# Kernel tuning notes

Hardware: AMD Instinct MI355X
Metric: run time of the kernel (lower is better)

## Reference

```python
import jax, jax.numpy as jnp
import numpy as np

B, T, C = 2, 2048, 1024
N_HEAD = 16
HEAD = C // N_HEAD  # 64


def setup_inputs() -> dict:
    key = jax.random.key(0)
    k1, k2, k3, k4, k5 = jax.random.split(key, 5)
    s = 1.0 / np.sqrt(C)
    return {
        "x": jax.random.normal(k1, (B, T, C), dtype=jnp.float32),
        "w_qkv": jax.random.normal(k2, (C, 3 * C), dtype=jnp.float32) * s,
        "b_qkv": jax.random.normal(k3, (3 * C,), dtype=jnp.float32) * 0.01,
        "w_proj": jax.random.normal(k4, (C, C), dtype=jnp.float32) * s,
        "b_proj": jax.random.normal(k5, (C,), dtype=jnp.float32) * 0.01,
    }


def reference(x, w_qkv, b_qkv, w_proj, b_proj):
    b, t, c = x.shape
    # QKV projection -> (3, B, H, T, head)
    qkv = (x @ w_qkv + b_qkv).reshape(b, t, 3, N_HEAD, HEAD).transpose(2, 0, 3, 1, 4)
    q, k, v = qkv[0], qkv[1], qkv[2]
    # scaled causal attention scores [B,H,T,T]
    att = jnp.einsum("bhqd,bhkd->bhqk", q, k) * (HEAD ** -0.5)
    causal = jnp.tril(jnp.ones((t, t), dtype=bool))
    att = jnp.where(causal, att, jnp.float32(-jnp.inf))
    att = jax.nn.softmax(att, axis=-1)
    out = jnp.einsum("bhqk,bhkd->bhqd", att, v)  # [B,H,T,head]
    out = out.transpose(0, 2, 1, 3).reshape(b, t, c)
    # dropout is identity in eval mode (p effectively 0)
    return out @ w_proj + b_proj
```

## Files before the change

kernel.cpp:

```cpp
#include <hip/hip_runtime.h>
#include <cstdint>

typedef __attribute__((ext_vector_type(8))) short bf16x8_t;
typedef __attribute__((ext_vector_type(4))) float f32x4_t;
typedef __attribute__((ext_vector_type(16))) float f32x16_t;

#define T_SEQ 2048
#define NHEAD 16
#define CDIM  1024

__device__ __forceinline__ unsigned short f2bf(float f) {
  union { float f; unsigned u; } v; v.f = f;
  unsigned r = v.u + 0x7FFFu + ((v.u >> 16) & 1u);
  return (unsigned short)(r >> 16);
}

__device__ __forceinline__ float fast_exp2(float x) {
#if __has_builtin(__builtin_amdgcn_exp2f)
  return __builtin_amdgcn_exp2f(x);
#else
  return __expf(x * 0.6931471805599453f);
#endif
}

__device__ __forceinline__ unsigned cvtpk(float lo, float hi) {
  unsigned r;
  asm("v_cvt_pk_bf16_f32 %0, %1, %2" : "=v"(r) : "v"(lo), "v"(hi));
  return r;
}
#define PLSWAP(a, b) asm("v_permlane32_swap_b32 %0, %1" : "+v"(a), "+v"(b))

__device__ __forceinline__ void gload_lds16(const void* g, void* l) {
  typedef const uint32_t __attribute__((address_space(1)))* gp_t;
  typedef uint32_t __attribute__((address_space(3)))* lp_t;
  __builtin_amdgcn_global_load_lds((gp_t)(uintptr_t)g, (lp_t)(uint32_t)(uintptr_t)l, 16, 0, 0);
}

__global__ void conv_bf16_kernel(const float* __restrict__ in,
                                 unsigned short* __restrict__ out, int n4) {
  int i = blockIdx.x * blockDim.x + threadIdx.x;
  if (i >= n4) return;
  float4 v = ((const float4*)in)[i];
  ushort4 o;
  o.x = f2bf(v.x); o.y = f2bf(v.y); o.z = f2bf(v.z); o.w = f2bf(v.w);
  ((ushort4*)out)[i] = o;
}

__global__ void transpose_bf16_kernel(const float* __restrict__ W,
                                      unsigned short* __restrict__ WT, int R, int C) {
  __shared__ unsigned short tile[64][65];
  const int c0 = blockIdx.x * 64, r0 = blockIdx.y * 64;
  const int t = threadIdx.x;
  #pragma unroll
  for (int i = 0; i < 16; i++) {
    int idx = i * 256 + t;
    int r = idx >> 6, c = idx & 63;
    tile[r][c] = f2bf(W[(size_t)(r0 + r) * C + c0 + c]);
  }
  __syncthreads();
  #pragma unroll
  for (int i = 0; i < 16; i++) {
    int idx = i * 256 + t;
    int c = idx >> 6, r = idx & 63;
    WT[(size_t)(c0 + c) * R + r0 + r] = tile[r][c];
  }
}

template <int MODE>
__global__ void gemm_bt_kernel(const unsigned short* __restrict__ A,
                               const unsigned short* __restrict__ Bt,
                               const float* __restrict__ bias,
                               unsigned short* __restrict__ q_out,
                               unsigned short* __restrict__ k_out,
                               unsigned short* __restrict__ v_out,
                               float* __restrict__ c_out,
                               int K, int N) {
  const int t = threadIdx.x;
  const int w = t >> 6, l = t & 63;
  const int lr = l & 15, lg = l >> 4;
  const int wr = w >> 1, wc = w & 1;
  const int m0 = blockIdx.y * 128, n0 = blockIdx.x * 128;

  __shared__ __align__(16) unsigned short As[128 * 64];
  __shared__ __align__(16) unsigned short Bs[128 * 64];

  f32x4_t acc[4][4];
  #pragma unroll
  for (int mi = 0; mi < 4; mi++)
    #pragma unroll
    for (int ni = 0; ni < 4; ni++)
      acc[mi][ni] = (f32x4_t){0.f, 0.f, 0.f, 0.f};

  const int srow = t >> 3;
  const int scol = (t & 7) * 8;
  const size_t abase = (size_t)(m0 + srow) * K + scol;
  const size_t bbase = (size_t)(n0 + srow) * K + scol;

  for (int k0 = 0; k0 < K; k0 += 64) {
    __syncthreads();
    #pragma unroll
    for (int i = 0; i < 4; i++) {
      gload_lds16(A + abase + (size_t)i * 32 * K + k0, &As[(i * 32 + srow) * 64 + scol]);
      gload_lds16(Bt + bbase + (size_t)i * 32 * K + k0, &Bs[(i * 32 + srow) * 64 + scol]);
    }
    __syncthreads();
    #pragma unroll
    for (int ks = 0; ks < 2; ks++) {
      bf16x8_t af[4], bfr[4];
      #pragma unroll
      for (int mi = 0; mi < 4; mi++)
        af[mi] = *(const bf16x8_t*)&As[(wr * 64 + mi * 16 + lr) * 64 + ks * 32 + lg * 8];
      #pragma unroll
      for (int ni = 0; ni < 4; ni++)
        bfr[ni] = *(const bf16x8_t*)&Bs[(wc * 64 + ni * 16 + lr) * 64 + ks * 32 + lg * 8];
      #pragma unroll
      for (int mi = 0; mi < 4; mi++)
        #pragma unroll
        for (int ni = 0; ni < 4; ni++)
          acc[mi][ni] = __builtin_amdgcn_mfma_f32_16x16x32_bf16(af[mi], bfr[ni], acc[mi][ni], 0, 0, 0);
    }
  }

  if (MODE == 0) {
    const float QSCALE = 0.125f * 1.4426950408889634f;
    #pragma unroll
    for (int ni = 0; ni < 4; ni++) {
      const int n = n0 + wc * 64 + ni * 16 + lr;
      const float bv = bias[n];
      const int s = n >> 10;
      const int hh = (n >> 6) & 15;
      const int d = n & 63;
      #pragma unroll
      for (int mi = 0; mi < 4; mi++) {
        const int mbase = m0 + wr * 64 + mi * 16 + lg * 4;
        const int batch = mbase >> 11;
        const int tt = mbase & 2047;
        const int bhh = batch * NHEAD + hh;
        if (s == 0) {
          #pragma unroll
          for (int r = 0; r < 4; r++)
            q_out[((size_t)bhh * T_SEQ + tt + r) * 64 + d] = f2bf((acc[mi][ni][r] + bv) * QSCALE);
        } else if (s == 1) {
          #pragma unroll
          for (int r = 0; r < 4; r++) {
            const int dsw = ((((d >> 3) ^ ((tt + r) & 7)) << 3) | (d & 7));
            k_out[((size_t)bhh * T_SEQ + tt + r) * 64 + dsw] = f2bf(acc[mi][ni][r] + bv);
          }
        } else {
          ushort4 pk;
          pk.x = f2bf(acc[mi][ni][0] + bv);
          pk.y = f2bf(acc[mi][ni][1] + bv);
          pk.z = f2bf(acc[mi][ni][2] + bv);
          pk.w = f2bf(acc[mi][ni][3] + bv);
          const int c2 = (((tt >> 3) & 7) ^ (d & 7));
          const int tt2 = (tt & ~63) | (c2 << 3) | (tt & 7);
          *(ushort4*)&v_out[((size_t)bhh * 64 + d) * T_SEQ + tt2] = pk;
        }
      }
    }
  } else {
    #pragma unroll
    for (int ni = 0; ni < 4; ni++) {
      const int n = n0 + wc * 64 + ni * 16 + lr;
      const float bv = bias[n];
      #pragma unroll
      for (int mi = 0; mi < 4; mi++) {
        const int m = m0 + wr * 64 + mi * 16 + lg * 4;
        #pragma unroll
        for (int r = 0; r < 4; r++)
          c_out[(size_t)(m + r) * N + n] = acc[mi][ni][r] + bv;
      }
    }
  }
}

__global__ __launch_bounds__(256, 2)
void attn_kernel(const unsigned short* __restrict__ Qb,
                 const unsigned short* __restrict__ Kswz,
                 const unsigned short* __restrict__ Vswz,
                 unsigned short* __restrict__ O) {
  const int b0 = blockIdx.x;
  const int xcd = b0 & 7;
  const int i = b0 >> 3;
  const int bh = xcd * 4 + (i & 3);
  const int strip = 15 - (i >> 2);
  const int batch = bh >> 4, h = bh & 15;
  const int q0 = strip * 128;
  const int nT = 2 * strip + 2;

  const int t = threadIdx.x;
  const int w = t >> 6, l = t & 63;
  const int q31 = l & 31, hi = l >> 5;

  __shared__ __align__(16) unsigned short Ks[2][64 * 64];
  __shared__ __align__(16) unsigned short Vs[2][64 * 64];

  const size_t kvbase = (size_t)bh * T_SEQ;

  auto stage = [&](int buf, int kv0) {
    #pragma unroll
    for (int i2 = 0; i2 < 2; i2++) {
      const int r0 = w * 16 + i2 * 8;
      gload_lds16(Kswz + (kvbase + kv0 + r0 + (l >> 3)) * 64 + (l & 7) * 8,
                  &Ks[buf][r0 * 64 + l * 8]);
      gload_lds16(Vswz + ((size_t)bh * 64 + r0 + (l >> 3)) * T_SEQ + kv0 + (l & 7) * 8,
                  &Vs[buf][r0 * 64 + l * 8]);
    }
  };

  bf16x8_t qf[4];
  #pragma unroll
  for (int ds = 0; ds < 4; ds++)
    qf[ds] = *(const bf16x8_t*)&Qb[(kvbase + q0 + w * 32 + q31) * 64 + ds * 16 + hi * 8];

  f32x16_t accO[2];
  #pragma unroll
  for (int di = 0; di < 2; di++)
    #pragma unroll
    for (int j = 0; j < 16; j++) accO[di][j] = 0.f;
  float l_part = 0.f;

  stage(0, 0);
  __syncthreads();
  int cur = 0;

  for (int ti = 0; ti < nT; ++ti) {
    if (ti + 1 < nT) stage(cur ^ 1, (ti + 1) * 64);

    const bool active = !(ti == nT - 1 && w < 2);
    if (active) {
      f32x16_t sc[2];
      #pragma unroll
      for (int c = 0; c < 2; c++)
        #pragma unroll
        for (int j = 0; j < 16; j++) sc[c][j] = 0.f;
      #pragma unroll
      for (int ds = 0; ds < 4; ds++) {
        #pragma unroll
        for (int c = 0; c < 2; c++) {
          const int row = c * 32 + q31;
          bf16x8_t ka = *(const bf16x8_t*)&Ks[cur][row * 64 + (((ds * 2 + hi) ^ (row & 7)) << 3)];
          sc[c] = __builtin_amdgcn_mfma_f32_32x32x16_bf16(ka, qf[ds], sc[c], 0, 0, 0);
        }
      }

      if ((ti == nT - 2 && w < 2) || (ti == nT - 1 && w >= 2)) {
        const int lb = (ti == nT - 1) ? 64 : 0;
        const int ql = w * 32 + q31;
        #pragma unroll
        for (int c = 0; c < 2; c++)
          #pragma unroll
          for (int r = 0; r < 16; r++) {
            const int kvl = lb + c * 32 + (r & 3) + 8 * (r >> 2) + 4 * hi;
            if (kvl > ql) sc[c][r] = -1e30f;
          }
      }

      #pragma unroll
      for (int c = 0; c < 2; c++) {
        float p[16];
        #pragma unroll
        for (int r = 0; r < 16; r++) {
          p[r] = fast_exp2(sc[c][r]);
          l_part += p[r];
        }
        unsigned pk0 = cvtpk(p[0], p[1]),   pk1 = cvtpk(p[2], p[3]);
        unsigned pk2 = cvtpk(p[4], p[5]),   pk3 = cvtpk(p[6], p[7]);
        unsigned pk4 = cvtpk(p[8], p[9]),   pk5 = cvtpk(p[10], p[11]);
        unsigned pk6 = cvtpk(p[12], p[13]), pk7 = cvtpk(p[14], p[15]);

        PLSWAP(pk0, pk2);
        PLSWAP(pk1, pk3);
        union { unsigned u[4]; bf16x8_t v; } pb0 = {{pk0, pk1, pk2, pk3}};
        {
          const int s = c * 2;
          #pragma unroll
          for (int di = 0; di < 2; di++) {
            const int row = di * 32 + q31;
            bf16x8_t va = *(const bf16x8_t*)&Vs[cur][row * 64 + (((s * 2 + hi) ^ (row & 7)) << 3)];
            accO[di] = __builtin_amdgcn_mfma_f32_32x32x16_bf16(va, pb0.v, accO[di], 0, 0, 0);
          }
        }
        PLSWAP(pk4, pk6);
        PLSWAP(pk5, pk7);
        union { unsigned u[4]; bf16x8_t v; } pb1 = {{pk4, pk5, pk6, pk7}};
        {
          const int s = c * 2 + 1;
          #pragma unroll
          for (int di = 0; di < 2; di++) {
            const int row = di * 32 + q31;
            bf16x8_t va = *(const bf16x8_t*)&Vs[cur][row * 64 + (((s * 2 + hi) ^ (row & 7)) << 3)];
            accO[di] = __builtin_amdgcn_mfma_f32_32x32x16_bf16(va, pb1.v, accO[di], 0, 0, 0);
          }
        }
      }
    }

    __syncthreads();
    cur ^= 1;
  }

  const float l_tot = l_part + __shfl_xor(l_part, 32);
  const float rl = 1.0f / l_tot;
  const int q = q0 + w * 32 + q31;
  unsigned short* orow = O + ((size_t)batch * T_SEQ + q) * CDIM + h * 64;
  #pragma unroll
  for (int di = 0; di < 2; di++)
    #pragma unroll
    for (int g = 0; g < 4; g++) {
      const unsigned w0 = cvtpk(accO[di][4 * g] * rl, accO[di][4 * g + 1] * rl);
      const unsigned w1 = cvtpk(accO[di][4 * g + 2] * rl, accO[di][4 * g + 3] * rl);
      const int d = di * 32 + 8 * g + 4 * hi;
      uint2 pr; pr.x = w0; pr.y = w1;
      *(uint2*)&orow[d] = pr;
    }
}

extern "C" void kernel_launch(void* const* d_in, const int* in_sizes, int n_in,
                              void* d_out, int out_size, void* d_ws, size_t ws_size,
                              hipStream_t stream) {
  (void)in_sizes; (void)n_in; (void)out_size; (void)ws_size;
  const float* x      = (const float*)d_in[0];
  const float* w_qkv  = (const float*)d_in[1];
  const float* b_qkv  = (const float*)d_in[2];
  const float* w_proj = (const float*)d_in[3];
  const float* b_proj = (const float*)d_in[4];
  float* out = (float*)d_out;

  char* ws = (char*)d_ws;
  unsigned short* xb     = (unsigned short*)(ws);
  unsigned short* wqkvT  = (unsigned short*)(ws + ((size_t)8  << 20));
  unsigned short* wprojT = (unsigned short*)(ws + ((size_t)14 << 20));
  unsigned short* qb     = (unsigned short*)(ws + ((size_t)16 << 20));
  unsigned short* kb     = (unsigned short*)(ws + ((size_t)24 << 20));
  unsigned short* vtb    = (unsigned short*)(ws + ((size_t)32 << 20));
  unsigned short* ab     = (unsigned short*)(ws + ((size_t)40 << 20));

  conv_bf16_kernel<<<4096, 256, 0, stream>>>(x, xb, (2 * T_SEQ * CDIM) / 4);
  transpose_bf16_kernel<<<dim3(48, 16), 256, 0, stream>>>(w_qkv, wqkvT, 1024, 3072);
  transpose_bf16_kernel<<<dim3(16, 16), 256, 0, stream>>>(w_proj, wprojT, 1024, 1024);
  gemm_bt_kernel<0><<<dim3(24, 32), 256, 0, stream>>>(xb, wqkvT, b_qkv, qb, kb, vtb, nullptr, 1024, 3072);
  attn_kernel<<<512, 256, 0, stream>>>(qb, kb, vtb, ab);
  gemm_bt_kernel<1><<<dim3(8, 32), 256, 0, stream>>>(ab, wprojT, b_proj, nullptr, nullptr, nullptr, out, 1024, 1024);
}
```

Before: 109.2 us.

## Shrink GEMM tiles, remap blocks per XCD, and raise occupancy

The QKV GEMM now uses 128x64 tiles and the output projection uses 64x64 tiles, replacing 128x128. Blocks are launched on a 1-D grid and remapped so each XCD works on a contiguous band of rows, which should improve L2 reuse. Launch bounds ask for higher occupancy and K is fixed at compile time. The aim is more blocks in flight and better latency hiding across the 256 CUs. The cost is less data reuse per tile and more redundant loads of the A and B tiles.

Measured after the change: 110.5 us. Within noise of the previous version (+1.1%).

```diff
diff --git a/kernel.cpp b/kernel.cpp
--- a/kernel.cpp
+++ b/kernel.cpp
@@ -67,28 +67,43 @@
 }
 
 template <int MODE>
-__global__ void gemm_bt_kernel(const unsigned short* __restrict__ A,
-                               const unsigned short* __restrict__ Bt,
-                               const float* __restrict__ bias,
-                               unsigned short* __restrict__ q_out,
-                               unsigned short* __restrict__ k_out,
-                               unsigned short* __restrict__ v_out,
-                               float* __restrict__ c_out,
-                               int K, int N) {
+__global__ __launch_bounds__(256, MODE == 0 ? 6 : 4)
+void gemm_bt_kernel(const unsigned short* __restrict__ A,
+                    const unsigned short* __restrict__ Bt,
+                    const float* __restrict__ bias,
+                    unsigned short* __restrict__ q_out,
+                    unsigned short* __restrict__ k_out,
+                    unsigned short* __restrict__ v_out,
+                    float* __restrict__ c_out) {
+  constexpr int TM = (MODE == 0) ? 128 : 64;
+  constexpr int FM = TM / 32;
+  constexpr int K = 1024;
+
   const int t = threadIdx.x;
   const int w = t >> 6, l = t & 63;
   const int lr = l & 15, lg = l >> 4;
   const int wr = w >> 1, wc = w & 1;
-  const int m0 = blockIdx.y * 128, n0 = blockIdx.x * 128;
-
-  __shared__ __align__(16) unsigned short As[128 * 64];
-  __shared__ __align__(16) unsigned short Bs[128 * 64];
-
-  f32x4_t acc[4][4];
-  #pragma unroll
-  for (int mi = 0; mi < 4; mi++)
-    #pragma unroll
-    for (int ni = 0; ni < 4; ni++)
+
+  const int b0 = blockIdx.x;
+  const int xcd = b0 & 7;
+  const int idx = b0 >> 3;
+  int m0, n0;
+  if (MODE == 0) {
+    m0 = (xcd * 4 + idx / 48) * 128;
+    n0 = (idx % 48) * 64;
+  } else {
+    m0 = (xcd * 8 + (idx >> 4)) * 64;
+    n0 = (idx & 15) * 64;
+  }
+
+  __shared__ __align__(16) unsigned short As[TM * 64];
+  __shared__ __align__(16) unsigned short Bs[64 * 64];
+
+  f32x4_t acc[FM][2];
+  #pragma unroll
+  for (int mi = 0; mi < FM; mi++)
+    #pragma unroll
+    for (int ni = 0; ni < 2; ni++)
       acc[mi][ni] = (f32x4_t){0.f, 0.f, 0.f, 0.f};
 
   const int srow = t >> 3;
@@ -99,24 +114,25 @@
   for (int k0 = 0; k0 < K; k0 += 64) {
     __syncthreads();
     #pragma unroll
-    for (int i = 0; i < 4; i++) {
+    for (int i = 0; i < TM / 32; i++)
       gload_lds16(A + abase + (size_t)i * 32 * K + k0, &As[(i * 32 + srow) * 64 + scol]);
+    #pragma unroll
+    for (int i = 0; i < 2; i++)
       gload_lds16(Bt + bbase + (size_t)i * 32 * K + k0, &Bs[(i * 32 + srow) * 64 + scol]);
-    }
     __syncthreads();
     #pragma unroll
     for (int ks = 0; ks < 2; ks++) {
-      bf16x8_t af[4], bfr[4];
-      #pragma unroll
-      for (int mi = 0; mi < 4; mi++)
-        af[mi] = *(const bf16x8_t*)&As[(wr * 64 + mi * 16 + lr) * 64 + ks * 32 + lg * 8];
-      #pragma unroll
-      for (int ni = 0; ni < 4; ni++)
-        bfr[ni] = *(const bf16x8_t*)&Bs[(wc * 64 + ni * 16 + lr) * 64 + ks * 32 + lg * 8];
-      #pragma unroll
-      for (int mi = 0; mi < 4; mi++)
-        #pragma unroll
-        for (int ni = 0; ni < 4; ni++)
+      bf16x8_t af[FM], bfr[2];
+      #pragma unroll
+      for (int mi = 0; mi < FM; mi++)
+        af[mi] = *(const bf16x8_t*)&As[(wr * (TM / 2) + mi * 16 + lr) * 64 + ks * 32 + lg * 8];
+      #pragma unroll
+      for (int ni = 0; ni < 2; ni++)
+        bfr[ni] = *(const bf16x8_t*)&Bs[(wc * 32 + ni * 16 + lr) * 64 + ks * 32 + lg * 8];
+      #pragma unroll
+      for (int mi = 0; mi < FM; mi++)
+        #pragma unroll
+        for (int ni = 0; ni < 2; ni++)
           acc[mi][ni] = __builtin_amdgcn_mfma_f32_16x16x32_bf16(af[mi], bfr[ni], acc[mi][ni], 0, 0, 0);
     }
   }
@@ -124,14 +140,14 @@
   if (MODE == 0) {
     const float QSCALE = 0.125f * 1.4426950408889634f;
     #pragma unroll
-    for (int ni = 0; ni < 4; ni++) {
-      const int n = n0 + wc * 64 + ni * 16 + lr;
+    for (int ni = 0; ni < 2; ni++) {
+      const int n = n0 + wc * 32 + ni * 16 + lr;
       const float bv = bias[n];
       const int s = n >> 10;
       const int hh = (n >> 6) & 15;
       const int d = n & 63;
       #pragma unroll
-      for (int mi = 0; mi < 4; mi++) {
+      for (int mi = 0; mi < FM; mi++) {
         const int mbase = m0 + wr * 64 + mi * 16 + lg * 4;
         const int batch = mbase >> 11;
         const int tt = mbase & 2047;
@@ -160,15 +176,15 @@
     }
   } else {
     #pragma unroll
-    for (int ni = 0; ni < 4; ni++) {
-      const int n = n0 + wc * 64 + ni * 16 + lr;
+    for (int ni = 0; ni < 2; ni++) {
+      const int n = n0 + wc * 32 + ni * 16 + lr;
       const float bv = bias[n];
       #pragma unroll
-      for (int mi = 0; mi < 4; mi++) {
-        const int m = m0 + wr * 64 + mi * 16 + lg * 4;
+      for (int mi = 0; mi < FM; mi++) {
+        const int m = m0 + wr * 32 + mi * 16 + lg * 4;
         #pragma unroll
         for (int r = 0; r < 4; r++)
-          c_out[(size_t)(m + r) * N + n] = acc[mi][ni][r] + bv;
+          c_out[(size_t)(m + r) * 1024 + n] = acc[mi][ni][r] + bv;
       }
     }
   }
@@ -339,7 +355,7 @@
   conv_bf16_kernel<<<4096, 256, 0, stream>>>(x, xb, (2 * T_SEQ * CDIM) / 4);
   transpose_bf16_kernel<<<dim3(48, 16), 256, 0, stream>>>(w_qkv, wqkvT, 1024, 3072);
   transpose_bf16_kernel<<<dim3(16, 16), 256, 0, stream>>>(w_proj, wprojT, 1024, 1024);
-  gemm_bt_kernel<0><<<dim3(24, 32), 256, 0, stream>>>(xb, wqkvT, b_qkv, qb, kb, vtb, nullptr, 1024, 3072);
+  gemm_bt_kernel<0><<<1536, 256, 0, stream>>>(xb, wqkvT, b_qkv, qb, kb, vtb, nullptr);
   attn_kernel<<<512, 256, 0, stream>>>(qb, kb, vtb, ab);
-  gemm_bt_kernel<1><<<dim3(8, 32), 256, 0, stream>>>(ab, wprojT, b_proj, nullptr, nullptr, nullptr, out, 1024, 1024);
-}
+  gemm_bt_kernel<1><<<1024, 256, 0, stream>>>(ab, wprojT, b_proj, nullptr, nullptr, nullptr, out);
+}
```
